# Performance work log

Hardware: AMD Instinct MI355X
Metric: run time of the kernel (lower is better)

## Reference

```python
import jax, jax.numpy as jnp
import numpy as np

B, S, D = 16, 2048, 128


def setup_inputs() -> dict:
    k = jax.random.key(0)
    k1, k2, k3, k4 = jax.random.split(k, 4)
    query = jax.random.normal(k1, (B, S, D), dtype=jnp.float32)
    key = jax.random.normal(k2, (B, S, D), dtype=jnp.float32)
    value = jax.random.normal(k3, (B, S, D), dtype=jnp.float32)
    # per-query tensor-valued inverse scale; shift away from zero for stable division
    inv_scale_factor = jax.random.uniform(k4, (B, S, 1), dtype=jnp.float32) + 0.5
    dropout_p = jnp.float32(0.1)
    return {"query": query, "key": key, "value": value,
            "inv_scale_factor": inv_scale_factor, "dropout_p": dropout_p}


def reference(query, key, value, inv_scale_factor, dropout_p):
    # QK^T: [B, Sq, Sk]
    qk = jnp.einsum('bqd,bkd->bqk', query, key)
    # tensor-valued scale divide (broadcast [B, Sq, 1] over keys)
    scaled_qk = qk / inv_scale_factor
    softmax_qk = jax.nn.softmax(scaled_qk, axis=-1)
    # dropout with a fixed RNG key (deterministic reference)
    keep_prob = 1.0 - dropout_p
    mask = jax.random.bernoulli(jax.random.key(42), keep_prob, softmax_qk.shape)
    dropout_qk = jnp.where(mask, softmax_qk / keep_prob, jnp.float32(0.0))
    # AV: [B, Sq, Dv]
    return jnp.einsum('bqk,bkv->bqv', dropout_qk, value)
```

## Files before the change

### kernel.cpp

```cpp
#include <hip/hip_runtime.h>
#include <hip/hip_bf16.h>
#include <stdint.h>


#define B_ 16
#define S_ 2048
#define D_ 128
#define TQ 64
#define TK 64
#define KSTR 136
#define VSTR 72
#define PSTR 72

typedef float f32x4 __attribute__((ext_vector_type(4)));
typedef short b16x8 __attribute__((ext_vector_type(8)));

union U4B8 { uint32_t u[4]; b16x8 v; };
union F32R { float4 q[8]; float f[32]; };
union F16R { float4 q[4]; float f[16]; };

__device__ __forceinline__ uint32_t pk_bf16(float a, float b) {
  union { __hip_bfloat162 h; uint32_t u; } c;
  c.h = __float22bfloat162_rn(make_float2(a, b));
  return c.u;
}

__device__ __forceinline__ uint2 threefry2x32_0_42(uint32_t x0, uint32_t x1) {
  const uint32_t k0 = 0u, k1 = 42u;
  const uint32_t k2 = 0x1BD11BDAu ^ k0 ^ k1;
  x0 += k0; x1 += k1;
#define TFR(r) { x0 += x1; x1 = (x1 << (r)) | (x1 >> (32 - (r))); x1 ^= x0; }
  TFR(13) TFR(15) TFR(26) TFR(6)
  x0 += k1; x1 += k2 + 1u;
  TFR(17) TFR(29) TFR(16) TFR(24)
  x0 += k2; x1 += k0 + 2u;
  TFR(13) TFR(15) TFR(26) TFR(6)
  x0 += k0; x1 += k1 + 3u;
  TFR(17) TFR(29) TFR(16) TFR(24)
  x0 += k1; x1 += k2 + 4u;
  TFR(13) TFR(15) TFR(26) TFR(6)
  x0 += k2; x1 += k0 + 5u;
#undef TFR
  return make_uint2(x0, x1);
}

__device__ __forceinline__ uint32_t jax_bits(uint32_t j) {
  const uint2 tf = threefry2x32_0_42(0u, j);
  return tf.x ^ tf.y;
}

__global__ __launch_bounds__(256, 2)
void attn_mfma_kernel(const float* __restrict__ Q, const float* __restrict__ K,
                      const float* __restrict__ V, const float* __restrict__ ISF,
                      const float* __restrict__ DP, float* __restrict__ OUT) {
  __shared__ __align__(16) short sKhi[TK * KSTR];
  __shared__ __align__(16) short sKlo[TK * KSTR];
  __shared__ __align__(16) short sVT[D_ * VSTR];
  __shared__ __align__(16) short sP[4 * 16 * PSTR];

  const int t    = threadIdx.x;
  const int w    = t >> 6;
  const int lane = t & 63;
  const int l15  = lane & 15;
  const int quad = lane >> 4;
  const int b    = blockIdx.y;
  const int qw   = blockIdx.x * TQ + w * 16;

  const float kp = 1.0f - DP[0];
  const uint32_t TH = __float_as_uint(1.0f + kp) & 0x7FFFFFu;

  float m_[4], l_[4];
  uint32_t jq[4];
  #pragma unroll
  for (int r = 0; r < 4; ++r) {
    m_[r] = -INFINITY;
    l_[r] = 0.0f;
    jq[r] = ((uint32_t)b << 22) + (uint32_t)(qw + quad * 4 + r) * (uint32_t)S_;
  }

  b16x8 qhi[4], qlo[4];
  {
    const float qs = 1.0f / ISF[b * S_ + qw + l15];
    const float* qp = Q + ((size_t)(b * S_ + qw + l15)) * D_;
    #pragma unroll
    for (int c = 0; c < 4; ++c) {
      const float4 a = *(const float4*)(qp + c * 32 + quad * 8);
      const float4 d = *(const float4*)(qp + c * 32 + quad * 8 + 4);
      float xs[8] = {a.x, a.y, a.z, a.w, d.x, d.y, d.z, d.w};
      U4B8 hi, lo;
      #pragma unroll
      for (int p = 0; p < 4; ++p) {
        const float x0 = xs[2 * p] * qs, x1 = xs[2 * p + 1] * qs;
        const uint32_t h = pk_bf16(x0, x1);
        const float r0 = x0 - __uint_as_float(h << 16);
        const float r1 = x1 - __uint_as_float(h & 0xFFFF0000u);
        hi.u[p] = h;
        lo.u[p] = pk_bf16(r0, r1);
      }
      qhi[c] = hi.v;
      qlo[c] = lo.v;
    }
  }

  f32x4 accO[8];
  #pragma unroll
  for (int i = 0; i < 8; ++i) accO[i] = (f32x4){0.f, 0.f, 0.f, 0.f};

  short* const pwv = &sP[w * 16 * PSTR];

  const int krow = t >> 2, kcol = (t & 3) * 32;
  const int vkey = 2 * (t & 31), vseg = (t >> 5) * 16;

  F32R kreg;
  F16R vreg0, vreg1;

#define ISSUE_LOADS(KT)                                                        \
  {                                                                            \
    const float4* gk4 = (const float4*)(K +                                    \
        ((size_t)(b * S_ + (KT) * TK + krow)) * D_ + kcol);                    \
    _Pragma("unroll") for (int i = 0; i < 8; ++i) kreg.q[i] = gk4[i];          \
    const float4* gv4 = (const float4*)(V +                                    \
        ((size_t)(b * S_ + (KT) * TK + vkey)) * D_ + vseg);                    \
    _Pragma("unroll") for (int i = 0; i < 4; ++i) {                            \
      vreg0.q[i] = gv4[i];                                                     \
      vreg1.q[i] = gv4[i + 32];                \
    }                                                                          \
  }

  ISSUE_LOADS(0)

  for (int kt = 0; kt < S_ / TK; ++kt) {
    __syncthreads();

    {
      short* kh = &sKhi[krow * KSTR + kcol];
      short* kl = &sKlo[krow * KSTR + kcol];
      #pragma unroll
      for (int g = 0; g < 4; ++g) {
        U4B8 hi, lo;
        #pragma unroll
        for (int p = 0; p < 4; ++p) {
          const float x0 = kreg.f[g * 8 + 2 * p], x1 = kreg.f[g * 8 + 2 * p + 1];
          const uint32_t h = pk_bf16(x0, x1);
          const float r0 = x0 - __uint_as_float(h << 16);
          const float r1 = x1 - __uint_as_float(h & 0xFFFF0000u);
          hi.u[p] = h;
          lo.u[p] = pk_bf16(r0, r1);
        }
        *(b16x8*)&kh[g * 8] = hi.v;
        *(b16x8*)&kl[g * 8] = lo.v;
      }
    }
    {
      #pragma unroll
      for (int d = 0; d < 16; ++d)
        *(uint32_t*)&sVT[(vseg + d) * VSTR + vkey] = pk_bf16(vreg0.f[d], vreg1.f[d]);
    }
    __syncthreads();

    if (kt + 1 < S_ / TK) ISSUE_LOADS(kt + 1)

    f32x4 s[4];
    #pragma unroll
    for (int n = 0; n < 4; ++n) {
      f32x4 acc = (f32x4){0.f, 0.f, 0.f, 0.f};
      #pragma unroll
      for (int c = 0; c < 4; ++c) {
        const b16x8 bh = *(const b16x8*)&sKhi[(n * 16 + l15) * KSTR + c * 32 + quad * 8];
        const b16x8 bl = *(const b16x8*)&sKlo[(n * 16 + l15) * KSTR + c * 32 + quad * 8];
        acc = __builtin_amdgcn_mfma_f32_16x16x32_bf16(qhi[c], bh, acc, 0, 0, 0);
        acc = __builtin_amdgcn_mfma_f32_16x16x32_bf16(qhi[c], bl, acc, 0, 0, 0);
        acc = __builtin_amdgcn_mfma_f32_16x16x32_bf16(qlo[c], bh, acc, 0, 0, 0);
      }
      s[n] = acc;
    }

    float mx[4];
    #pragma unroll
    for (int r = 0; r < 4; ++r)
      mx[r] = fmaxf(fmaxf(s[0][r], s[1][r]), fmaxf(s[2][r], s[3][r]));
    #pragma unroll
    for (int off = 1; off < 16; off <<= 1) {
      #pragma unroll
      for (int r = 0; r < 4; ++r) mx[r] = fmaxf(mx[r], __shfl_xor(mx[r], off, 16));
    }
    float alpha[4], rs[4];
    #pragma unroll
    for (int r = 0; r < 4; ++r) {
      const float mnew = fmaxf(m_[r], mx[r]);
      alpha[r] = __expf(m_[r] - mnew);
      m_[r] = mnew;
      rs[r] = 0.f;
    }
    #pragma unroll
    for (int n = 0; n < 4; ++n) {
      #pragma unroll
      for (int r = 0; r < 4; ++r) {
        const float p = __expf(s[n][r] - m_[r]);
        s[n][r] = p;
        rs[r] += p;
      }
    }
    #pragma unroll
    for (int off = 1; off < 16; off <<= 1) {
      #pragma unroll
      for (int r = 0; r < 4; ++r) rs[r] += __shfl_xor(rs[r], off, 16);
    }
    #pragma unroll
    for (int r = 0; r < 4; ++r) l_[r] = l_[r] * alpha[r] + rs[r];
    #pragma unroll
    for (int i = 0; i < 8; ++i) {
      #pragma unroll
      for (int r = 0; r < 4; ++r) accO[i][r] *= alpha[r];
    }

    #pragma unroll
    for (int n = 0; n < 4; ++n) {
      const int col = n * 16 + l15;
      const uint32_t jcol = (uint32_t)(kt * TK + col);
      float pf[4];
      #pragma unroll
      for (int r = 0; r < 4; ++r) {
        const uint32_t bits = jax_bits(jq[r] + jcol);
        pf[r] = ((bits >> 9) < TH) ? s[n][r] : 0.0f;
      }
      const uint32_t pk01 = pk_bf16(pf[0], pf[1]);
      const uint32_t pk23 = pk_bf16(pf[2], pf[3]);
      pwv[(quad * 4 + 0) * PSTR + col] = (short)(uint16_t)pk01;
      pwv[(quad * 4 + 1) * PSTR + col] = (short)(uint16_t)(pk01 >> 16);
      pwv[(quad * 4 + 2) * PSTR + col] = (short)(uint16_t)pk23;
      pwv[(quad * 4 + 3) * PSTR + col] = (short)(uint16_t)(pk23 >> 16);
    }
    __threadfence_block();

    #pragma unroll
    for (int ks = 0; ks < 2; ++ks) {
      const b16x8 ap = *(const b16x8*)&pwv[l15 * PSTR + ks * 32 + quad * 8];
      #pragma unroll
      for (int d8 = 0; d8 < 8; ++d8) {
        const b16x8 bv = *(const b16x8*)&sVT[(d8 * 16 + l15) * VSTR + ks * 32 + quad * 8];
        accO[d8] = __builtin_amdgcn_mfma_f32_16x16x32_bf16(ap, bv, accO[d8], 0, 0, 0);
      }
    }
  }
#undef ISSUE_LOADS

  float inv[4];
  #pragma unroll
  for (int r = 0; r < 4; ++r) inv[r] = 1.0f / (l_[r] * kp);
  float* op = OUT + ((size_t)(b * S_ + qw)) * D_;
  #pragma unroll
  for (int d8 = 0; d8 < 8; ++d8) {
    #pragma unroll
    for (int r = 0; r < 4; ++r)
      op[(quad * 4 + r) * D_ + d8 * 16 + l15] = accO[d8][r] * inv[r];
  }
}

extern "C" void kernel_launch(void* const* d_in, const int* in_sizes, int n_in,
                              void* d_out, int out_size, void* d_ws, size_t ws_size,
                              hipStream_t stream) {
  const float* q   = (const float*)d_in[0];
  const float* k   = (const float*)d_in[1];
  const float* v   = (const float*)d_in[2];
  const float* isf = (const float*)d_in[3];
  const float* dp  = (const float*)d_in[4];
  float* out = (float*)d_out;

  dim3 grid(S_ / TQ, B_);
  attn_mfma_kernel<<<grid, dim3(256), 0, stream>>>(q, k, v, isf, dp, out);
}
```

Measured before the change: 342.4 us.

## Use DPP row reductions, exp2 softmax, and skip rescale when max unchanged

Replaces the shuffle-based 16-lane max and sum reductions with DPP row-rotate reductions. Folds log2(e) into the query scale so the softmax can use native exp2. It also skips the accumulator rescale when no row max grows, uses a rotate builtin in threefry, and compares the dropout bits against a pre-shifted threshold. These cut ALU and cross-lane work in the softmax and RNG path, adding a wave-uniform branch and relying on the DPP row-rotate semantics.

```diff
diff --git a/kernel.cpp b/kernel.cpp
--- a/kernel.cpp
+++ b/kernel.cpp
@@ -25,11 +25,28 @@
   return c.u;
 }
 
+#define DPP_ROR(x, ctrl) \
+  __int_as_float(__builtin_amdgcn_update_dpp(0, __float_as_int(x), (ctrl), 0xf, 0xf, true))
+__device__ __forceinline__ float row16_max(float x) {
+  x = fmaxf(x, DPP_ROR(x, 0x128));
+  x = fmaxf(x, DPP_ROR(x, 0x124));
+  x = fmaxf(x, DPP_ROR(x, 0x122));
+  x = fmaxf(x, DPP_ROR(x, 0x121));
+  return x;
+}
+__device__ __forceinline__ float row16_sum(float x) {
+  x += DPP_ROR(x, 0x128);
+  x += DPP_ROR(x, 0x124);
+  x += DPP_ROR(x, 0x122);
+  x += DPP_ROR(x, 0x121);
+  return x;
+}
+
 __device__ __forceinline__ uint2 threefry2x32_0_42(uint32_t x0, uint32_t x1) {
   const uint32_t k0 = 0u, k1 = 42u;
   const uint32_t k2 = 0x1BD11BDAu ^ k0 ^ k1;
   x0 += k0; x1 += k1;
-#define TFR(r) { x0 += x1; x1 = (x1 << (r)) | (x1 >> (32 - (r))); x1 ^= x0; }
+#define TFR(r) { x0 += x1; x1 = __builtin_rotateleft32(x1, r); x1 ^= x0; }
   TFR(13) TFR(15) TFR(26) TFR(6)
   x0 += k1; x1 += k2 + 1u;
   TFR(17) TFR(29) TFR(16) TFR(24)
@@ -67,7 +84,7 @@
   const int qw   = blockIdx.x * TQ + w * 16;
 
   const float kp = 1.0f - DP[0];
-  const uint32_t TH = __float_as_uint(1.0f + kp) & 0x7FFFFFu;
+  const uint32_t TH9 = (__float_as_uint(1.0f + kp) & 0x7FFFFFu) << 9;
 
   float m_[4], l_[4];
   uint32_t jq[4];
@@ -80,7 +97,7 @@
 
   b16x8 qhi[4], qlo[4];
   {
-    const float qs = 1.0f / ISF[b * S_ + qw + l15];
+    const float qs = 1.4426950408889634f / ISF[b * S_ + qw + l15];
     const float* qp = Q + ((size_t)(b * S_ + qw + l15)) * D_;
     #pragma unroll
     for (int c = 0; c < 4; ++c) {
@@ -177,42 +194,37 @@
 
     float mx[4];
     #pragma unroll
-    for (int r = 0; r < 4; ++r)
-      mx[r] = fmaxf(fmaxf(s[0][r], s[1][r]), fmaxf(s[2][r], s[3][r]));
-    #pragma unroll
-    for (int off = 1; off < 16; off <<= 1) {
-      #pragma unroll
-      for (int r = 0; r < 4; ++r) mx[r] = fmaxf(mx[r], __shfl_xor(mx[r], off, 16));
-    }
-    float alpha[4], rs[4];
-    #pragma unroll
     for (int r = 0; r < 4; ++r) {
-      const float mnew = fmaxf(m_[r], mx[r]);
-      alpha[r] = __expf(m_[r] - mnew);
-      m_[r] = mnew;
-      rs[r] = 0.f;
-    }
-    #pragma unroll
-    for (int n = 0; n < 4; ++n) {
+      mx[r] = row16_max(fmaxf(fmaxf(s[0][r], s[1][r]), fmaxf(s[2][r], s[3][r])));
+    }
+    int changed = 0;
+    #pragma unroll
+    for (int r = 0; r < 4; ++r) changed |= (mx[r] > m_[r]);
+    if (__ballot(changed) != 0ull) {
       #pragma unroll
       for (int r = 0; r < 4; ++r) {
-        const float p = __expf(s[n][r] - m_[r]);
+        const float mnew = fmaxf(m_[r], mx[r]);
+        const float alpha = __builtin_amdgcn_exp2f(m_[r] - mnew);
+        m_[r] = mnew;
+        l_[r] *= alpha;
+        #pragma unroll
+        for (int i = 0; i < 8; ++i) accO[i][r] *= alpha;
+      }
+    }
+    float rs[4];
+    #pragma unroll
+    for (int r = 0; r < 4; ++r) {
+      float lr = 0.f;
+      #pragma unroll
+      for (int n = 0; n < 4; ++n) {
+        const float p = __builtin_amdgcn_exp2f(s[n][r] - m_[r]);
         s[n][r] = p;
-        rs[r] += p;
-      }
-    }
-    #pragma unroll
-    for (int off = 1; off < 16; off <<= 1) {
-      #pragma unroll
-      for (int r = 0; r < 4; ++r) rs[r] += __shfl_xor(rs[r], off, 16);
-    }
-    #pragma unroll
-    for (int r = 0; r < 4; ++r) l_[r] = l_[r] * alpha[r] + rs[r];
-    #pragma unroll
-    for (int i = 0; i < 8; ++i) {
-      #pragma unroll
-      for (int r = 0; r < 4; ++r) accO[i][r] *= alpha[r];
-    }
+        lr += p;
+      }
+      rs[r] = lr;
+    }
+    #pragma unroll
+    for (int r = 0; r < 4; ++r) l_[r] += row16_sum(rs[r]);
 
     #pragma unroll
     for (int n = 0; n < 4; ++n) {
@@ -222,7 +234,7 @@
       #pragma unroll
       for (int r = 0; r < 4; ++r) {
         const uint32_t bits = jax_bits(jq[r] + jcol);
-        pf[r] = ((bits >> 9) < TH) ? s[n][r] : 0.0f;
+        pf[r] = (bits < TH9) ? s[n][r] : 0.0f;
       }
       const uint32_t pk01 = pk_bf16(pf[0], pf[1]);
       const uint32_t pk23 = pk_bf16(pf[2], pf[3]);
```

After: 330.7 us. 3.4% less time.
